# Optimization experiments

Hardware: AMD Instinct MI355X
Metric: run time of the kernel (lower is better)

## Reference

```python
import jax, jax.numpy as jnp
import numpy as np

N_USER = 1_000_000
N_ITEM = 100_000
E = 16          # embedding_size
O = 16          # out_size per head
H = 4           # head_num
HID = 32        # hidden_size
B = 8192        # batch
S = 200         # sample_num
L = 50          # history length
NSUPP = 50_000  # supp_user_num


def _xavier(key, shape):
    fan_in, fan_out = shape[-2], shape[-1]
    std = np.sqrt(2.0 / (fan_in + fan_out))
    return (jax.random.normal(key, shape) * std).astype(jnp.float32)


def setup_inputs() -> dict:
    key = jax.random.key(0)
    ks = jax.random.split(key, 16)
    uid = jax.random.randint(ks[0], (B,), 0, N_USER)
    iid = jax.random.randint(ks[1], (B,), 0, N_ITEM)
    return {
        "user_embedding": _xavier(ks[2], (N_USER, E)),
        "item_embedding": _xavier(ks[3], (N_ITEM, E)),
        "wq": _xavier(ks[4], (H, E, O)),   # per-head Wq (no bias)
        "wk": _xavier(ks[5], (H, E, O)),
        "wv": _xavier(ks[6], (H, O, O)),
        "w_out": _xavier(ks[7], (H * O, O)),
        "l1_w": _xavier(ks[8], (3 * E, HID)),
        "l1_b": jnp.full((HID,), 0.1, jnp.float32),
        "l2_w": _xavier(ks[9], (HID, HID // 2)),
        "l2_b": jnp.full((HID // 2,), 0.1, jnp.float32),
        "l3_w": _xavier(ks[10], (HID // 2, 1)),
        "l3_b": jnp.full((1,), 0.1, jnp.float32),
        "user_bias": jnp.zeros((N_USER, 1), jnp.float32),
        "item_bias": jnp.zeros((N_ITEM, 1), jnp.float32),
        "x": jnp.stack([uid, iid], axis=1),                          # [B,2]
        "history": jax.random.randint(ks[11], (B, L), 0, N_ITEM),    # [B,L]
        "history_len": jax.random.randint(ks[12], (B,), 1, L + 1),   # [B] >=1
        "supp_users": jax.random.randint(ks[13], (NSUPP,), 0, N_USER),
        "sample_index": jax.random.randint(ks[14], (H, B, S), 0, NSUPP),
    }


def reference(user_embedding, item_embedding, wq, wk, wv, w_out,
              l1_w, l1_b, l2_w, l2_b, l3_w, l3_b, user_bias, item_bias,
              x, history, history_len, supp_users, sample_index):
    user_id = x[:, 0]
    item_id = x[:, 1]

    # user init embedding = mean-by-len of full (unmasked) history, as in source
    hist_emb = item_embedding[history]                                # [B,L,E]
    user_init = hist_emb.sum(axis=1) / history_len[:, None].astype(jnp.float32)  # [B,E]

    # per-head GAT over sampled support users (all heads vectorized)
    nb = user_embedding[supp_users[sample_index]]                     # [H,B,S,E]
    q = jnp.einsum('be,heo->hbo', user_init, wq)                      # [H,B,O]
    k = jnp.einsum('hbse,heo->hbso', nb, wk)                          # [H,B,S,O]
    attn = jax.nn.softmax(jnp.einsum('hbo,hbso->hbs', q, k), axis=-1)
    ctx = jnp.einsum('hbs,hbso->hbo', attn, k)                        # [H,B,O]
    gat = jnp.einsum('hbo,hop->hbp', ctx, wv)                         # [H,B,O]
    gat = jnp.transpose(gat, (1, 0, 2)).reshape(B, H * O)             # concat heads

    user_emb = gat @ w_out                                            # [B,O]
    item_emb = item_embedding[item_id]                                # [B,E]
    interaction = user_emb * item_emb
    ratings = interaction.sum(axis=1)

    h = jnp.concatenate([user_emb, item_emb, interaction], axis=1)    # [B,3E]
    x1 = jnp.tanh(h @ l1_w + l1_b)
    x2 = jnp.tanh(x1 @ l2_w + l2_b)
    x3 = (x2 @ l3_w + l3_b).reshape(-1)

    ub = user_bias[user_id, 0]
    ib = item_bias[item_id, 0]
    return (ratings + x3) / 2.0 + ub + ib
```

## Files before the change

### kernel.cpp

```cpp
#include <hip/hip_runtime.h>
#include <math.h>

#define N_USERS 1000000
#define N_ITEMS 100000
#define EMB 16
#define OUTD 16
#define NH 4
#define HID 32
#define BB 8192
#define SS 200
#define LL 50
#define NSUPP 50000

__global__ __launch_bounds__(256) void k_supp_kernel(
    const float* __restrict__ user_emb,
    const int*   __restrict__ supp_users,
    const float* __restrict__ wk,
    float*       __restrict__ Ksupp)
{
    __shared__ float s_wk[NH * EMB * OUTD];
    __shared__ float s_u[16][EMB];
    int t = threadIdx.x;
    for (int i = t; i < NH * EMB * OUTD; i += 256) s_wk[i] = wk[i];
    int n0 = blockIdx.x * 16;
    {
        int ul = t >> 4, e = t & 15;
        int row = supp_users[n0 + ul];
        s_u[ul][e] = user_emb[(size_t)row * EMB + e];
    }
    __syncthreads();
    int h   = t >> 6;
    int sub = (t >> 4) & 3;
    int o   = t & 15;
#pragma unroll
    for (int r = 0; r < 4; ++r) {
        int ul = sub + 4 * r;
        float acc = 0.f;
#pragma unroll
        for (int e = 0; e < EMB; ++e)
            acc += s_u[ul][e] * s_wk[(h * EMB + e) * OUTD + o];
        Ksupp[((size_t)h * NSUPP + n0 + ul) * OUTD + o] = acc;
    }
}

__global__ __launch_bounds__(256) void user_init_q_kernel(
    const float* __restrict__ item_emb,
    const int*   __restrict__ history,
    const int*   __restrict__ history_len,
    const float* __restrict__ wq,
    float*       __restrict__ qbuf)
{
    __shared__ float s_ui[4][EMB];
    __shared__ float s_wq[NH * EMB * OUTD];
    int t = threadIdx.x;
    for (int i = t; i < NH * EMB * OUTD; i += 256) s_wq[i] = wq[i];

    int g    = t >> 6;
    int lane = t & 63;
    int l4   = lane >> 4;
    int e    = lane & 15;
    int b    = blockIdx.x * 4 + g;

    float sum = 0.f;
    for (int l = l4; l < LL; l += 4) {
        int it = history[(size_t)b * LL + l];
        sum += item_emb[(size_t)it * EMB + e];
    }
    sum += __shfl_xor(sum, 16);
    sum += __shfl_xor(sum, 32);
    if (lane < EMB) s_ui[g][lane] = sum / (float)history_len[b];
    __syncthreads();

    int g2 = t >> 6;
    int h  = (t >> 4) & 3;
    int o  = t & 15;
    int b2 = blockIdx.x * 4 + g2;
    float acc = 0.f;
#pragma unroll
    for (int ee = 0; ee < EMB; ++ee)
        acc += s_ui[g2][ee] * s_wq[(h * EMB + ee) * OUTD + o];
    qbuf[((size_t)b2 * NH + h) * OUTD + o] = acc;
}

__global__ __launch_bounds__(256) void attn_kernel(
    const float* __restrict__ Ksupp,
    const float* __restrict__ qbuf,
    const int*   __restrict__ sample_index,
    const float* __restrict__ wv,
    float*       __restrict__ gat)
{
    int blk   = blockIdx.x;
    int h     = (blk & 7) >> 1;
    int btile = ((blk >> 3) << 1) | (blk & 1);
    int wave  = threadIdx.x >> 6;
    int lane  = threadIdx.x & 63;
    int b     = btile * 4 + wave;

    float q[EMB];
    const float* qp = qbuf + ((size_t)b * NH + h) * OUTD;
#pragma unroll
    for (int e = 0; e < EMB; ++e) q[e] = qp[e];

    const int*   si = sample_index + ((size_t)h * BB + b) * SS;
    const float* Kh = Ksupp + (size_t)h * NSUPP * OUTD;

    float m = -3.0e38f, l = 0.f;
    float c[OUTD];
#pragma unroll
    for (int e = 0; e < OUTD; ++e) c[e] = 0.f;

#pragma unroll
    for (int i = 0; i < 4; ++i) {
        int s = lane + 64 * i;
        if (s < SS) {
            int idx = si[s];
            const float4* kp = reinterpret_cast<const float4*>(Kh + (size_t)idx * OUTD);
            float4 a0 = kp[0], a1 = kp[1], a2 = kp[2], a3 = kp[3];
            float k[OUTD] = {a0.x,a0.y,a0.z,a0.w, a1.x,a1.y,a1.z,a1.w,
                             a2.x,a2.y,a2.z,a2.w, a3.x,a3.y,a3.z,a3.w};
            float d = 0.f;
#pragma unroll
            for (int e = 0; e < EMB; ++e) d += q[e] * k[e];
            float mn = fmaxf(m, d);
            float sc = __expf(m - mn);
            float w  = __expf(d - mn);
            l = l * sc + w;
#pragma unroll
            for (int e = 0; e < OUTD; ++e) c[e] = c[e] * sc + w * k[e];
            m = mn;
        }
    }

#pragma unroll
    for (int off = 32; off; off >>= 1) {
        float m2 = __shfl_xor(m, off);
        float l2 = __shfl_xor(l, off);
        float mn = fmaxf(m, m2);
        float a  = __expf(m - mn);
        float bb = __expf(m2 - mn);
        l = l * a + l2 * bb;
#pragma unroll
        for (int e = 0; e < OUTD; ++e) {
            float c2 = __shfl_xor(c[e], off);
            c[e] = c[e] * a + c2 * bb;
        }
        m = mn;
    }

    float inv = 1.f / l;
    if (lane < OUTD) {
        float g = 0.f;
#pragma unroll
        for (int o = 0; o < OUTD; ++o)
            g += c[o] * wv[(h * OUTD + o) * OUTD + lane];
        gat[(size_t)b * (NH * OUTD) + h * OUTD + lane] = g * inv;
    }
}

__global__ __launch_bounds__(256) void epilogue_kernel(
    const float* __restrict__ gat,
    const float* __restrict__ item_emb,
    const float* __restrict__ w_out,
    const float* __restrict__ l1_w, const float* __restrict__ l1_b,
    const float* __restrict__ l2_w, const float* __restrict__ l2_b,
    const float* __restrict__ l3_w, const float* __restrict__ l3_b,
    const float* __restrict__ user_bias, const float* __restrict__ item_bias,
    const int*   __restrict__ x,
    float*       __restrict__ out)
{
    int t    = threadIdx.x;
    int g    = t >> 6;
    int lane = t & 63;
    int b    = blockIdx.x * 4 + g;

    __shared__ float s_gat[4][NH * OUTD];
    __shared__ float s_ue[4][OUTD];
    __shared__ float s_ie[4][EMB];
    __shared__ float s_x1[4][HID];
    __shared__ float s_x2[4][HID / 2];

    int uid = x[(size_t)b * 2 + 0];
    int iid = x[(size_t)b * 2 + 1];

    s_gat[g][lane] = gat[(size_t)b * (NH * OUTD) + lane];
    if (lane < EMB) s_ie[g][lane] = item_emb[(size_t)iid * EMB + lane];
    __syncthreads();

    if (lane < OUTD) {
        float acc = 0.f;
#pragma unroll
        for (int j = 0; j < NH * OUTD; ++j) acc += s_gat[g][j] * w_out[j * OUTD + lane];
        s_ue[g][lane] = acc;
    }
    __syncthreads();

    if (lane < HID) {
        float acc = l1_b[lane];
#pragma unroll
        for (int i = 0; i < EMB; ++i) {
            float ue = s_ue[g][i], ie = s_ie[g][i];
            acc += ue * l1_w[i * HID + lane]
                 + ie * l1_w[(EMB + i) * HID + lane]
                 + ue * ie * l1_w[(2 * EMB + i) * HID + lane];
        }
        s_x1[g][lane] = tanhf(acc);
    }
    __syncthreads();

    if (lane < HID / 2) {
        float acc = l2_b[lane];
#pragma unroll
        for (int j = 0; j < HID; ++j) acc += s_x1[g][j] * l2_w[j * (HID / 2) + lane];
        s_x2[g][lane] = tanhf(acc);
    }
    __syncthreads();

    if (lane == 0) {
        float x3 = l3_b[0];
#pragma unroll
        for (int j = 0; j < HID / 2; ++j) x3 += s_x2[g][j] * l3_w[j];
        float ratings = 0.f;
#pragma unroll
        for (int o = 0; o < OUTD; ++o) ratings += s_ue[g][o] * s_ie[g][o];
        out[b] = 0.5f * (ratings + x3) + user_bias[uid] + item_bias[iid];
    }
}

extern "C" void kernel_launch(void* const* d_in, const int* in_sizes, int n_in,
                              void* d_out, int out_size, void* d_ws, size_t ws_size,
                              hipStream_t stream) {
    const float* user_embedding = (const float*)d_in[0];
    const float* item_embedding = (const float*)d_in[1];
    const float* wq             = (const float*)d_in[2];
    const float* wk             = (const float*)d_in[3];
    const float* wv             = (const float*)d_in[4];
    const float* w_out          = (const float*)d_in[5];
    const float* l1_w           = (const float*)d_in[6];
    const float* l1_b           = (const float*)d_in[7];
    const float* l2_w           = (const float*)d_in[8];
    const float* l2_b           = (const float*)d_in[9];
    const float* l3_w           = (const float*)d_in[10];
    const float* l3_b           = (const float*)d_in[11];
    const float* user_bias      = (const float*)d_in[12];
    const float* item_bias      = (const float*)d_in[13];
    const int*   x              = (const int*)d_in[14];
    const int*   history        = (const int*)d_in[15];
    const int*   history_len    = (const int*)d_in[16];
    const int*   supp_users     = (const int*)d_in[17];
    const int*   sample_index   = (const int*)d_in[18];
    float* out = (float*)d_out;

    char* ws = (char*)d_ws;
    float* Ksupp = (float*)ws;
    ws += (size_t)NH * NSUPP * OUTD * sizeof(float);
    float* qbuf  = (float*)ws;
    ws += (size_t)BB * NH * OUTD * sizeof(float);
    float* gat   = (float*)ws;

    k_supp_kernel<<<NSUPP / 16, 256, 0, stream>>>(user_embedding, supp_users, wk, Ksupp);
    user_init_q_kernel<<<BB / 4, 256, 0, stream>>>(item_embedding, history, history_len, wq, qbuf);
    attn_kernel<<<NH * BB / 4, 256, 0, stream>>>(Ksupp, qbuf, sample_index, wv, gat);
    epilogue_kernel<<<BB / 4, 256, 0, stream>>>(
        gat, item_embedding, w_out, l1_w, l1_b, l2_w, l2_b, l3_w, l3_b,
        user_bias, item_bias, x, out);
}
```

Before: 242.7 us.

## Split each attention row across 4 lanes with float4 loads and two-pass softmax

```diff
diff --git a/kernel.cpp b/kernel.cpp
--- a/kernel.cpp
+++ b/kernel.cpp
@@ -12,6 +12,8 @@
 #define LL 50
 #define NSUPP 50000
 
+typedef float v4f __attribute__((ext_vector_type(4)));
+
 __global__ __launch_bounds__(256) void k_supp_kernel(
     const float* __restrict__ user_emb,
     const int*   __restrict__ supp_users,
@@ -63,7 +65,7 @@
 
     float sum = 0.f;
     for (int l = l4; l < LL; l += 4) {
-        int it = history[(size_t)b * LL + l];
+        int it = __builtin_nontemporal_load(history + (size_t)b * LL + l);
         sum += item_emb[(size_t)it * EMB + e];
     }
     sum += __shfl_xor(sum, 16);
@@ -71,18 +73,16 @@
     if (lane < EMB) s_ui[g][lane] = sum / (float)history_len[b];
     __syncthreads();
 
-    int g2 = t >> 6;
     int h  = (t >> 4) & 3;
     int o  = t & 15;
-    int b2 = blockIdx.x * 4 + g2;
     float acc = 0.f;
 #pragma unroll
     for (int ee = 0; ee < EMB; ++ee)
-        acc += s_ui[g2][ee] * s_wq[(h * EMB + ee) * OUTD + o];
-    qbuf[((size_t)b2 * NH + h) * OUTD + o] = acc;
-}
-
-__global__ __launch_bounds__(256) void attn_kernel(
+        acc += s_ui[g][ee] * s_wq[(h * EMB + ee) * OUTD + o];
+    qbuf[((size_t)b * NH + h) * OUTD + o] = acc;
+}
+
+__global__ __launch_bounds__(256, 4) void attn_kernel(
     const float* __restrict__ Ksupp,
     const float* __restrict__ qbuf,
     const int*   __restrict__ sample_index,
@@ -95,66 +95,74 @@
     int wave  = threadIdx.x >> 6;
     int lane  = threadIdx.x & 63;
     int b     = btile * 4 + wave;
-
-    float q[EMB];
-    const float* qp = qbuf + ((size_t)b * NH + h) * OUTD;
-#pragma unroll
-    for (int e = 0; e < EMB; ++e) q[e] = qp[e];
-
-    const int*   si = sample_index + ((size_t)h * BB + b) * SS;
+    int g     = lane >> 2;
+    int qt    = lane & 3;
+
+    const int* si = sample_index + ((size_t)h * BB + b) * SS;
+    int pre0 = __builtin_nontemporal_load(si + lane);
+    int pre1 = __builtin_nontemporal_load(si + lane + 64);
+    int pre2 = __builtin_nontemporal_load(si + lane + 128);
+    int pre3 = (lane < 8) ? __builtin_nontemporal_load(si + lane + 192) : 0;
+
+    v4f qv = __builtin_nontemporal_load(
+        (const v4f*)(qbuf + ((size_t)b * NH + h) * OUTD) + qt);
+
     const float* Kh = Ksupp + (size_t)h * NSUPP * OUTD;
 
-    float m = -3.0e38f, l = 0.f;
-    float c[OUTD];
-#pragma unroll
-    for (int e = 0; e < OUTD; ++e) c[e] = 0.f;
-
-#pragma unroll
-    for (int i = 0; i < 4; ++i) {
-        int s = lane + 64 * i;
-        if (s < SS) {
-            int idx = si[s];
-            const float4* kp = reinterpret_cast<const float4*>(Kh + (size_t)idx * OUTD);
-            float4 a0 = kp[0], a1 = kp[1], a2 = kp[2], a3 = kp[3];
-            float k[OUTD] = {a0.x,a0.y,a0.z,a0.w, a1.x,a1.y,a1.z,a1.w,
-                             a2.x,a2.y,a2.z,a2.w, a3.x,a3.y,a3.z,a3.w};
-            float d = 0.f;
-#pragma unroll
-            for (int e = 0; e < EMB; ++e) d += q[e] * k[e];
-            float mn = fmaxf(m, d);
-            float sc = __expf(m - mn);
-            float w  = __expf(d - mn);
-            l = l * sc + w;
-#pragma unroll
-            for (int e = 0; e < OUTD; ++e) c[e] = c[e] * sc + w * k[e];
-            m = mn;
-        }
-    }
-
-#pragma unroll
-    for (int off = 32; off; off >>= 1) {
-        float m2 = __shfl_xor(m, off);
-        float l2 = __shfl_xor(l, off);
-        float mn = fmaxf(m, m2);
-        float a  = __expf(m - mn);
-        float bb = __expf(m2 - mn);
-        l = l * a + l2 * bb;
-#pragma unroll
-        for (int e = 0; e < OUTD; ++e) {
-            float c2 = __shfl_xor(c[e], off);
-            c[e] = c[e] * a + c2 * bb;
-        }
-        m = mn;
-    }
-
+    int idx[13];
+#pragma unroll
+    for (int r = 0; r < 13; ++r) {
+        int pre = (r < 4) ? pre0 : (r < 8) ? pre1 : (r < 12) ? pre2 : pre3;
+        idx[r] = __shfl(pre, (r & 3) * 16 + g, 64);
+    }
+
+    v4f kq[13];
+#pragma unroll
+    for (int r = 0; r < 13; ++r)
+        kq[r] = *(const v4f*)(Kh + (size_t)idx[r] * OUTD + qt * 4);
+
+    float d[13];
+#pragma unroll
+    for (int r = 0; r < 13; ++r) {
+        float p = kq[r].x * qv.x + kq[r].y * qv.y + kq[r].z * qv.z + kq[r].w * qv.w;
+        p += __shfl_xor(p, 1);
+        p += __shfl_xor(p, 2);
+        d[r] = p;
+    }
+    if (g >= 8) d[12] = -3.0e38f;
+
+    float m = d[0];
+#pragma unroll
+    for (int r = 1; r < 13; ++r) m = fmaxf(m, d[r]);
+#pragma unroll
+    for (int off = 4; off < 64; off <<= 1) m = fmaxf(m, __shfl_xor(m, off));
+
+    float l = 0.f;
+    v4f c = {0.f, 0.f, 0.f, 0.f};
+#pragma unroll
+    for (int r = 0; r < 13; ++r) {
+        float w = __expf(d[r] - m);
+        l += w;
+        c += w * kq[r];
+    }
+#pragma unroll
+    for (int off = 4; off < 64; off <<= 1) {
+        l   += __shfl_xor(l, off);
+        c.x += __shfl_xor(c.x, off);
+        c.y += __shfl_xor(c.y, off);
+        c.z += __shfl_xor(c.z, off);
+        c.w += __shfl_xor(c.w, off);
+    }
     float inv = 1.f / l;
-    if (lane < OUTD) {
-        float g = 0.f;
-#pragma unroll
-        for (int o = 0; o < OUTD; ++o)
-            g += c[o] * wv[(h * OUTD + o) * OUTD + lane];
-        gat[(size_t)b * (NH * OUTD) + h * OUTD + lane] = g * inv;
-    }
+
+    float part = c.x * wv[((size_t)h * OUTD + qt * 4 + 0) * OUTD + g]
+               + c.y * wv[((size_t)h * OUTD + qt * 4 + 1) * OUTD + g]
+               + c.z * wv[((size_t)h * OUTD + qt * 4 + 2) * OUTD + g]
+               + c.w * wv[((size_t)h * OUTD + qt * 4 + 3) * OUTD + g];
+    part += __shfl_xor(part, 1);
+    part += __shfl_xor(part, 2);
+    if (qt == 0)
+        gat[(size_t)b * (NH * OUTD) + h * OUTD + g] = part * inv;
 }
 
 __global__ __launch_bounds__(256) void epilogue_kernel(
```

Measured after the change: 214.0 us. -11.8%, faster.
